# Kernel tuning notes

Hardware: AMD Instinct MI355X
Metric: run time of the kernel (lower is better)

Reference implementation:

```python
import jax, jax.numpy as jnp
import numpy as np

B, L, D, H, NL = 4, 1024, 1024, 16, 4
Dh = D // H          # 64 head dim
DFF = 4 * D          # GLU FFN hidden
EPS = 1e-5
NVARS = 64


def setup_inputs() -> dict:
    key = jax.random.key(0)
    ks = jax.random.split(key, 12)
    init = lambda k, shape, s=0.02: jax.random.normal(k, shape, jnp.float32) * s
    return dict(
        x=jax.random.normal(ks[0], (B, L, D), jnp.float32),
        var_id=jax.random.randint(ks[1], (B, L), 0, NVARS),
        positions=jnp.sort(jax.random.randint(ks[2], (B, L), 0, L), axis=-1),
        Wqkv=init(ks[3], (NL, D, 3 * D)),
        Wo=init(ks[4], (NL, D, D)),
        norm1_w=jnp.ones((NL, D), jnp.float32),
        norm2_w=jnp.ones((NL, D), jnp.float32),
        q_norm_w=jnp.ones((NL, Dh), jnp.float32),
        k_norm_w=jnp.ones((NL, Dh), jnp.float32),
        bias_emb=init(ks[5], (NL, 2, H), 0.1),  # BinaryAttentionBias per layer
        W_gate=init(ks[6], (NL, D, DFF)),
        W_up=init(ks[7], (NL, D, DFF)),
        W_down=init(ks[8], (NL, DFF, D)),
        final_norm_w=jnp.ones((D,), jnp.float32),
    )


def reference(x, var_id, positions, Wqkv, Wo, norm1_w, norm2_w, q_norm_w,
              k_norm_w, bias_emb, W_gate, W_up, W_down, final_norm_w):
    # var-equality mask for BinaryAttentionBias: [B,1,L,L]
    same = (var_id[:, :, None] == var_id[:, None, :])[:, None]
    # partial RoPE: rotary on first half of head_dim (partial_factor (0.0, 0.5))
    rot = Dh // 2
    inv_freq = jnp.exp(-jnp.log(10000.0) * jnp.arange(0, rot, 2, dtype=jnp.float32) / rot)
    theta = positions.astype(jnp.float32)[..., None] * inv_freq  # [B,L,rot/2]
    cos = jnp.cos(theta)[:, :, None, :]  # [B,L,1,rot/2]
    sin = jnp.sin(theta)[:, :, None, :]

    def rmsnorm(t, w):
        return t * jax.lax.rsqrt(jnp.mean(t * t, -1, keepdims=True) + EPS) * w

    def rope(t):  # t: [B,L,H,Dh]
        tr, tp = t[..., :rot], t[..., rot:]
        t1, t2 = tr[..., 0::2], tr[..., 1::2]
        rr = jnp.stack([t1 * cos - t2 * sin, t1 * sin + t2 * cos], -1).reshape(tr.shape)
        return jnp.concatenate([rr, tp], -1)

    scale = 1.0 / np.sqrt(Dh).astype(np.float32)

    def layer(h, p):
        Wqkv_l, Wo_l, n1, n2, qn, kn, be, Wg, Wu, Wd = p
        y = rmsnorm(h, n1)
        qkv = y @ Wqkv_l  # [B,L,3D]
        q, k, v = [a.reshape(B, L, H, Dh) for a in jnp.split(qkv, 3, axis=-1)]
        q = rope(rmsnorm(q, qn))  # qk-norm then rotary
        k = rope(rmsnorm(k, kn))
        bias = jnp.where(same, be[1][None, :, None, None], be[0][None, :, None, None])
        scores = jnp.einsum('blhd,bmhd->bhlm', q, k) * scale + bias
        attn = jax.nn.softmax(scores, axis=-1)
        o = jnp.einsum('bhlm,bmhd->blhd', attn, v).reshape(B, L, D)
        h = h + o @ Wo_l
        y = rmsnorm(h, n2)
        h = h + (jax.nn.silu(y @ Wg) * (y @ Wu)) @ Wd  # SiLU-GLU FFN
        return h, None

    params = (Wqkv, Wo, norm1_w, norm2_w, q_norm_w, k_norm_w, bias_emb,
              W_gate, W_up, W_down)
    h, _ = jax.lax.scan(layer, x, params)
    return rmsnorm(h, final_norm_w)
```

## Files before the change

### kernel.cpp

```cpp
#include <hip/hip_runtime.h>
#include <hip/hip_bf16.h>
#include <math.h>

#define B_   4
#define L_   1024
#define D_   1024
#define H_   16
#define NL_  4
#define DH_  64
#define DFF_ 4096
#define EPS_ 1e-5f

typedef unsigned short u16;
typedef __attribute__((ext_vector_type(8))) short short8;
typedef __attribute__((ext_vector_type(4))) float f32x4;

static __device__ __forceinline__ u16 f2bf(float x) {
  union { float f; unsigned u; } c;
  c.f = x;
  unsigned r = c.u + 0x7fffu + ((c.u >> 16) & 1u);
  return (u16)(r >> 16);
}
static __device__ __forceinline__ float bf2f(u16 x) {
  union { unsigned u; float f; } c;
  c.u = ((unsigned)x) << 16;
  return c.f;
}

__global__ __launch_bounds__(256) void transpose_cast_kernel(
    const float* __restrict__ W, u16* __restrict__ Wt, int R, int C) {
  __shared__ float tile[64][65];
  int r0 = blockIdx.y * 64, c0 = blockIdx.x * 64;
  int t = threadIdx.x;
#pragma unroll
  for (int i = 0; i < 4; i++) {
    int f = t + i * 256;
    int rr = f >> 4, c4 = f & 15;
    float4 v = *(const float4*)(W + (size_t)(r0 + rr) * C + c0 + c4 * 4);
    tile[rr][c4 * 4 + 0] = v.x;
    tile[rr][c4 * 4 + 1] = v.y;
    tile[rr][c4 * 4 + 2] = v.z;
    tile[rr][c4 * 4 + 3] = v.w;
  }
  __syncthreads();
#pragma unroll
  for (int i = 0; i < 4; i++) {
    int f = t + i * 256;
    int cc = f >> 4, rq = f & 15;
    unsigned p0 = (unsigned)f2bf(tile[rq * 4 + 0][cc]) |
                  ((unsigned)f2bf(tile[rq * 4 + 1][cc]) << 16);
    unsigned p1 = (unsigned)f2bf(tile[rq * 4 + 2][cc]) |
                  ((unsigned)f2bf(tile[rq * 4 + 3][cc]) << 16);
    uint2 q; q.x = p0; q.y = p1;
    *(uint2*)(Wt + (size_t)(c0 + cc) * R + r0 + rq * 4) = q;
  }
}

__global__ __launch_bounds__(256) void rmsnorm_kernel(
    const float* __restrict__ in, const float* __restrict__ w,
    float* __restrict__ out) {
  int row = blockIdx.x;
  const float4* x4 = (const float4*)(in + (size_t)row * D_);
  float4* y4 = (float4*)(out + (size_t)row * D_);
  const float4* w4 = (const float4*)w;
  int t = threadIdx.x;
  float4 v = x4[t];
  float ss = v.x * v.x + v.y * v.y + v.z * v.z + v.w * v.w;
#pragma unroll
  for (int off = 32; off > 0; off >>= 1) ss += __shfl_down(ss, off, 64);
  __shared__ float red[4];
  if ((t & 63) == 0) red[t >> 6] = ss;
  __syncthreads();
  float tot = red[0] + red[1] + red[2] + red[3];
  float r = rsqrtf(tot * (1.0f / D_) + EPS_);
  float4 wv = w4[t];
  float4 o;
  o.x = v.x * r * wv.x;
  o.y = v.y * r * wv.y;
  o.z = v.z * r * wv.z;
  o.w = v.w * r * wv.w;
  y4[t] = o;
}

__global__ __launch_bounds__(256) void rmsnorm_bf16_kernel(
    const float* __restrict__ in, const float* __restrict__ w,
    u16* __restrict__ out) {
  int row = blockIdx.x;
  const float4* x4 = (const float4*)(in + (size_t)row * D_);
  const float4* w4 = (const float4*)w;
  int t = threadIdx.x;
  float4 v = x4[t];
  float ss = v.x * v.x + v.y * v.y + v.z * v.z + v.w * v.w;
#pragma unroll
  for (int off = 32; off > 0; off >>= 1) ss += __shfl_down(ss, off, 64);
  __shared__ float red[4];
  if ((t & 63) == 0) red[t >> 6] = ss;
  __syncthreads();
  float tot = red[0] + red[1] + red[2] + red[3];
  float r = rsqrtf(tot * (1.0f / D_) + EPS_);
  float4 wv = w4[t];
  unsigned p0 = (unsigned)f2bf(v.x * r * wv.x) |
                ((unsigned)f2bf(v.y * r * wv.y) << 16);
  unsigned p1 = (unsigned)f2bf(v.z * r * wv.z) |
                ((unsigned)f2bf(v.w * r * wv.w) << 16);
  uint2 q; q.x = p0; q.y = p1;
  *(uint2*)(out + (size_t)row * D_ + t * 4) = q;
}

__global__ __launch_bounds__(256) void qknorm_rope_kernel(
    u16* __restrict__ qkv, const int* __restrict__ positions,
    const float* __restrict__ qn, const float* __restrict__ kn) {
  int tok = blockIdx.x;
  int p = blockIdx.y * 4 + (threadIdx.x >> 6);
  int d = threadIdx.x & 63;
  int isK = p >> 4;
  int h = p & 15;
  const float* w = isK ? kn : qn;
  u16* ptr = qkv + (size_t)tok * (3 * D_) + (size_t)isK * D_ + h * 64;
  float v = bf2f(ptr[d]);
  float ss = v * v;
#pragma unroll
  for (int off = 1; off < 64; off <<= 1) ss += __shfl_xor(ss, off, 64);
  float r = rsqrtf(ss * (1.0f / 64.0f) + EPS_);
  v = v * r * w[d];
  float pv = __shfl_xor(v, 1, 64);
  float outv = v;
  if (d < 32) {
    int i = d >> 1;
    float freq = __expf(-logf(10000.0f) * (float)(2 * i) * (1.0f / 32.0f));
    float th = (float)positions[tok] * freq;
    float s, c;
    __sincosf(th, &s, &c);
    outv = (d & 1) ? (pv * s + v * c) : (v * c - pv * s);
  }
  ptr[d] = f2bf(outv);
}

template <int MODE>
__global__ __launch_bounds__(256) void gemm_mfma(
    const u16* __restrict__ A, const u16* __restrict__ Bt,
    void* __restrict__ C, int M, int N, int K) {
  __shared__ u16 As[4096];
  __shared__ u16 Bs[4096];
  int t = threadIdx.x;
  int lane = t & 63, wv = t >> 6;
  int wm = wv >> 1, wn = wv & 1;
  int m0 = blockIdx.y * 128, n0 = blockIdx.x * 128;
  int lm = lane & 15, lk = lane >> 4;
  f32x4 acc[4][4];
#pragma unroll
  for (int i = 0; i < 4; i++)
#pragma unroll
    for (int j = 0; j < 4; j++) acc[i][j] = (f32x4)0.0f;

  for (int k0 = 0; k0 < K; k0 += 32) {
#pragma unroll
    for (int i = 0; i < 2; i++) {
      int s = wv * 2 + i;
      const u16* g = A + (size_t)(m0 + s * 16 + lm) * K + k0 + lk * 8;
      __builtin_amdgcn_global_load_lds(
          (const __attribute__((address_space(1))) void*)g,
          (__attribute__((address_space(3))) void*)(As + s * 512), 16, 0, 0);
    }
#pragma unroll
    for (int i = 0; i < 2; i++) {
      int s = wv * 2 + i;
      const u16* g = Bt + (size_t)(n0 + s * 16 + lm) * K + k0 + lk * 8;
      __builtin_amdgcn_global_load_lds(
          (const __attribute__((address_space(1))) void*)g,
          (__attribute__((address_space(3))) void*)(Bs + s * 512), 16, 0, 0);
    }
    __syncthreads();
    short8 a[4], b[4];
#pragma unroll
    for (int i = 0; i < 4; i++)
      a[i] = *(const short8*)(As + (wm * 4 + i) * 512 + lane * 8);
#pragma unroll
    for (int j = 0; j < 4; j++)
      b[j] = *(const short8*)(Bs + (wn * 4 + j) * 512 + lane * 8);
#pragma unroll
    for (int i = 0; i < 4; i++)
#pragma unroll
      for (int j = 0; j < 4; j++)
        acc[i][j] = __builtin_amdgcn_mfma_f32_16x16x32_bf16(
            a[i], b[j], acc[i][j], 0, 0, 0);
    __syncthreads();
  }

  int rb = (lane >> 4) * 4;
  int cl = lane & 15;
  size_t colbase = (size_t)(n0 + wn * 64 + cl);
#pragma unroll
  for (int i = 0; i < 4; i++) {
#pragma unroll
    for (int r = 0; r < 4; r++) {
      size_t row = (size_t)(m0 + wm * 64 + i * 16 + rb + r);
      if (MODE == 0) {
        float* p = (float*)C + row * N + colbase;
#pragma unroll
        for (int j = 0; j < 4; j++) p[j * 16] = acc[i][j][r];
      } else if (MODE == 1) {
        float* p = (float*)C + row * N + colbase;
#pragma unroll
        for (int j = 0; j < 4; j++) p[j * 16] += acc[i][j][r];
      } else if (MODE == 2) {
        u16* p = (u16*)C + row * N + colbase;
#pragma unroll
        for (int j = 0; j < 4; j++) p[j * 16] = f2bf(acc[i][j][r]);
      } else {
        u16* p = (u16*)C + row * N + colbase;
#pragma unroll
        for (int j = 0; j < 4; j++) {
          float g = acc[i][j][r];
          float u = bf2f(p[j * 16]);
          float sv = g / (1.0f + __expf(-g));
          p[j * 16] = f2bf(sv * u);
        }
      }
    }
  }
}

__global__ __launch_bounds__(256) void attn_mfma_kernel(
    const u16* __restrict__ qkv, const int* __restrict__ var_id,
    const float* __restrict__ bias_l, u16* __restrict__ o) {
  __shared__ u16 Ps[4][16 * 72];
  __shared__ u16 Vt[64 * 72];
  __shared__ int vks[64];
  int b = blockIdx.z, h = blockIdx.y, q0 = blockIdx.x * 64;
  int t = threadIdx.x, lane = t & 63, w = t >> 6;
  int cl = lane & 15, qd = lane >> 4;
  const size_t ROW = 3 * D_;
  const u16* qbase = qkv + (size_t)(b * L_) * ROW + h * 64;
  const u16* kbase = qbase + D_;
  const u16* vbase = qbase + 2 * D_;
  const float scale = 0.125f;

  int qrow = q0 + w * 16 + cl;
  short8 aq0 = *(const short8*)(qbase + (size_t)qrow * ROW + qd * 8);
  short8 aq1 = *(const short8*)(qbase + (size_t)qrow * ROW + 32 + qd * 8);

  int vq[4];
#pragma unroll
  for (int r = 0; r < 4; r++)
    vq[r] = var_id[b * L_ + q0 + w * 16 + qd * 4 + r];
  float b0 = bias_l[h], b1 = bias_l[H_ + h];

  float m_i[4], l_i[4];
  f32x4 oc[4];
#pragma unroll
  for (int r = 0; r < 4; r++) { m_i[r] = -1e30f; l_i[r] = 0.0f; }
#pragma unroll
  for (int ds = 0; ds < 4; ds++) oc[ds] = (f32x4)0.0f;

  int kp = t & 31, g = t >> 5;

  for (int kt = 0; kt < 16; kt++) {
    int k0 = kt * 64;
    {
      const u16* v0 = vbase + (size_t)(k0 + 2 * kp) * ROW + g * 8;
      short8 va = *(const short8*)v0;
      short8 vb = *(const short8*)(v0 + ROW);
#pragma unroll
      for (int j = 0; j < 8; j++) {
        unsigned pk = (unsigned)(u16)va[j] | ((unsigned)(u16)vb[j] << 16);
        *(unsigned*)&Vt[(g * 8 + j) * 72 + 2 * kp] = pk;
      }
      if (t < 64) vks[t] = var_id[b * L_ + k0 + t];
    }
    __syncthreads();

    f32x4 s[4];
#pragma unroll
    for (int j = 0; j < 4; j++) {
      const u16* kr = kbase + (size_t)(k0 + j * 16 + cl) * ROW;
      short8 bk0 = *(const short8*)(kr + qd * 8);
      short8 bk1 = *(const short8*)(kr + 32 + qd * 8);
      f32x4 a = (f32x4)0.0f;
      a = __builtin_amdgcn_mfma_f32_16x16x32_bf16(aq0, bk0, a, 0, 0, 0);
      a = __builtin_amdgcn_mfma_f32_16x16x32_bf16(aq1, bk1, a, 0, 0, 0);
      s[j] = a;
    }
#pragma unroll
    for (int j = 0; j < 4; j++) {
      int kv = vks[j * 16 + cl];
#pragma unroll
      for (int r = 0; r < 4; r++)
        s[j][r] = s[j][r] * scale + ((kv == vq[r]) ? b1 : b0);
    }
#pragma unroll
    for (int r = 0; r < 4; r++) {
      float rm = fmaxf(fmaxf(s[0][r], s[1][r]), fmaxf(s[2][r], s[3][r]));
#pragma unroll
      for (int off = 1; off < 16; off <<= 1)
        rm = fmaxf(rm, __shfl_xor(rm, off, 64));
      float mnew = fmaxf(m_i[r], rm);
      float alpha = __expf(m_i[r] - mnew);
      m_i[r] = mnew;
      float rs = 0.0f;
#pragma unroll
      for (int j = 0; j < 4; j++) {
        float p = __expf(s[j][r] - mnew);
        s[j][r] = p;
        rs += p;
      }
#pragma unroll
      for (int off = 1; off < 16; off <<= 1) rs += __shfl_xor(rs, off, 64);
      l_i[r] = l_i[r] * alpha + rs;
#pragma unroll
      for (int ds = 0; ds < 4; ds++) oc[ds][r] *= alpha;
    }
#pragma unroll
    for (int j = 0; j < 4; j++)
#pragma unroll
      for (int r = 0; r < 4; r++)
        Ps[w][(qd * 4 + r) * 72 + j * 16 + cl] = f2bf(s[j][r]);

    short8 ap0 = *(const short8*)(&Ps[w][cl * 72 + qd * 8]);
    short8 ap1 = *(const short8*)(&Ps[w][cl * 72 + 32 + qd * 8]);
#pragma unroll
    for (int ds = 0; ds < 4; ds++) {
      const u16* vr = &Vt[(ds * 16 + cl) * 72];
      short8 bv0 = *(const short8*)(vr + qd * 8);
      short8 bv1 = *(const short8*)(vr + 32 + qd * 8);
      oc[ds] = __builtin_amdgcn_mfma_f32_16x16x32_bf16(ap0, bv0, oc[ds], 0, 0, 0);
      oc[ds] = __builtin_amdgcn_mfma_f32_16x16x32_bf16(ap1, bv1, oc[ds], 0, 0, 0);
    }
    __syncthreads();
  }

#pragma unroll
  for (int r = 0; r < 4; r++) {
    float inv = 1.0f / l_i[r];
    size_t row = (size_t)(b * L_ + q0 + w * 16 + qd * 4 + r);
#pragma unroll
    for (int ds = 0; ds < 4; ds++)
      o[row * D_ + h * 64 + ds * 16 + cl] = f2bf(oc[ds][r] * inv);
  }
}

extern "C" void kernel_launch(void* const* d_in, const int* in_sizes, int n_in,
                              void* d_out, int out_size, void* d_ws,
                              size_t ws_size, hipStream_t stream) {
  (void)in_sizes; (void)n_in; (void)out_size; (void)ws_size;
  const float* x    = (const float*)d_in[0];
  const int* var_id = (const int*)d_in[1];
  const int* pos    = (const int*)d_in[2];
  const float* Wqkv = (const float*)d_in[3];
  const float* Wo   = (const float*)d_in[4];
  const float* n1   = (const float*)d_in[5];
  const float* n2   = (const float*)d_in[6];
  const float* qn   = (const float*)d_in[7];
  const float* kn   = (const float*)d_in[8];
  const float* be   = (const float*)d_in[9];
  const float* Wg   = (const float*)d_in[10];
  const float* Wu   = (const float*)d_in[11];
  const float* Wd   = (const float*)d_in[12];
  const float* fnw  = (const float*)d_in[13];

  float* h = (float*)d_out;
  const size_t MB = 1u << 20;
  char* wsb = (char*)d_ws;
  u16* y   = (u16*)(wsb);
  u16* qkv = (u16*)(wsb + 8*MB);
  u16* o   = (u16*)(wsb + 24*MB);
  u16* ff  = (u16*)(wsb + 32*MB);
  u16* wT  = (u16*)(wsb + 64*MB);
  u16* wqkvT = wT;
  u16* woT   = wqkvT + (size_t)3072*1024;
  u16* wgT   = woT   + (size_t)1024*1024;
  u16* wuT   = wgT   + (size_t)4096*1024;
  u16* wdT   = wuT   + (size_t)4096*1024;

  const size_t SZ = (size_t)B_ * L_ * D_;
  hipMemcpyAsync(h, x, SZ * sizeof(float), hipMemcpyDeviceToDevice, stream);

  const int M = B_ * L_;
  for (int l = 0; l < NL_; l++) {
    transpose_cast_kernel<<<dim3(48, 16), 256, 0, stream>>>(
        Wqkv + (size_t)l * D_ * 3 * D_, wqkvT, D_, 3 * D_);
    transpose_cast_kernel<<<dim3(16, 16), 256, 0, stream>>>(
        Wo + (size_t)l * D_ * D_, woT, D_, D_);
    transpose_cast_kernel<<<dim3(64, 16), 256, 0, stream>>>(
        Wg + (size_t)l * D_ * DFF_, wgT, D_, DFF_);
    transpose_cast_kernel<<<dim3(64, 16), 256, 0, stream>>>(
        Wu + (size_t)l * D_ * DFF_, wuT, D_, DFF_);
    transpose_cast_kernel<<<dim3(16, 64), 256, 0, stream>>>(
        Wd + (size_t)l * DFF_ * D_, wdT, DFF_, D_);

    rmsnorm_bf16_kernel<<<M, 256, 0, stream>>>(h, n1 + (size_t)l * D_, y);
    gemm_mfma<2><<<dim3(3 * D_ / 128, M / 128), 256, 0, stream>>>(
        y, wqkvT, qkv, M, 3 * D_, D_);
    qknorm_rope_kernel<<<dim3(M, 8), 256, 0, stream>>>(
        qkv, pos, qn + (size_t)l * DH_, kn + (size_t)l * DH_);
    attn_mfma_kernel<<<dim3(L_ / 64, H_, B_), 256, 0, stream>>>(
        qkv, var_id, be + (size_t)l * 2 * H_, o);
    gemm_mfma<1><<<dim3(D_ / 128, M / 128), 256, 0, stream>>>(
        o, woT, h, M, D_, D_);
    rmsnorm_bf16_kernel<<<M, 256, 0, stream>>>(h, n2 + (size_t)l * D_, y);
    gemm_mfma<2><<<dim3(DFF_ / 128, M / 128), 256, 0, stream>>>(
        y, wuT, ff, M, DFF_, D_);
    gemm_mfma<3><<<dim3(DFF_ / 128, M / 128), 256, 0, stream>>>(
        y, wgT, ff, M, DFF_, D_);
    gemm_mfma<1><<<dim3(D_ / 128, M / 128), 256, 0, stream>>>(
        ff, wdT, h, M, D_, DFF_);
  }
  rmsnorm_kernel<<<M, 256, 0, stream>>>(h, fnw, h);
}
```

Measured before the change: 2.295 ms.

## Register-prefetch GEMM tiles, fuse gate/up FFN GEMMs, shrink M-tile for narrow GEMMs

The GEMM kernel now loads the next K-slice into registers while the current slice is in LDS, replacing direct global-to-LDS loads, so memory latency overlaps with MFMA work. The gate and up projections are fused into one kernel that shares the A tile and applies SiLU*up in the epilogue, removing the second pass over y and the read-modify-write of ff. The N=1024 GEMMs (Wo, Wdown) use 64-row M tiles to launch more blocks. Costs are more registers (two 4x4 accumulator sets in the fused kernel) and possibly lower occupancy.

After: 4.411 ms. +92.2%, slower.

```diff
diff --git a/kernel.cpp b/kernel.cpp
--- a/kernel.cpp
+++ b/kernel.cpp
@@ -136,86 +136,190 @@
   ptr[d] = f2bf(outv);
 }
 
-template <int MODE>
+template <int MODE, int AI>
 __global__ __launch_bounds__(256) void gemm_mfma(
     const u16* __restrict__ A, const u16* __restrict__ Bt,
     void* __restrict__ C, int M, int N, int K) {
+  const int NA = AI / 2;
+  __shared__ u16 As[AI * 1024];
+  __shared__ u16 Bs[4096];
+  int t = threadIdx.x;
+  int lane = t & 63, wv = t >> 6;
+  int wm = wv >> 1, wn = wv & 1;
+  int m0 = blockIdx.y * (AI * 32), n0 = blockIdx.x * 128;
+  int lm = lane & 15, lk = lane >> 4;
+
+  const u16* pa[NA];
+  const u16* pb[2];
+#pragma unroll
+  for (int i = 0; i < NA; i++)
+    pa[i] = A + (size_t)(m0 + (wv * NA + i) * 16 + lm) * K + lk * 8;
+#pragma unroll
+  for (int i = 0; i < 2; i++)
+    pb[i] = Bt + (size_t)(n0 + (wv * 2 + i) * 16 + lm) * K + lk * 8;
+
+  uint4 ca[NA], cb[2];
+#pragma unroll
+  for (int i = 0; i < NA; i++) ca[i] = *(const uint4*)pa[i];
+#pragma unroll
+  for (int i = 0; i < 2; i++) cb[i] = *(const uint4*)pb[i];
+
+  f32x4 acc[AI][4];
+#pragma unroll
+  for (int i = 0; i < AI; i++)
+#pragma unroll
+    for (int j = 0; j < 4; j++) acc[i][j] = (f32x4)0.0f;
+
+  for (int k0 = 0; k0 < K; k0 += 32) {
+#pragma unroll
+    for (int i = 0; i < NA; i++)
+      *(uint4*)(As + (wv * NA + i) * 512 + lane * 8) = ca[i];
+#pragma unroll
+    for (int i = 0; i < 2; i++)
+      *(uint4*)(Bs + (wv * 2 + i) * 512 + lane * 8) = cb[i];
+    int kn = (k0 + 32 < K) ? (k0 + 32) : 0;
+    uint4 na[NA], nb[2];
+#pragma unroll
+    for (int i = 0; i < NA; i++) na[i] = *(const uint4*)(pa[i] + kn);
+#pragma unroll
+    for (int i = 0; i < 2; i++) nb[i] = *(const uint4*)(pb[i] + kn);
+    __syncthreads();
+    short8 a[AI], b[4];
+#pragma unroll
+    for (int i = 0; i < AI; i++)
+      a[i] = *(const short8*)(As + (wm * AI + i) * 512 + lane * 8);
+#pragma unroll
+    for (int j = 0; j < 4; j++)
+      b[j] = *(const short8*)(Bs + (wn * 4 + j) * 512 + lane * 8);
+#pragma unroll
+    for (int i = 0; i < AI; i++)
+#pragma unroll
+      for (int j = 0; j < 4; j++)
+        acc[i][j] = __builtin_amdgcn_mfma_f32_16x16x32_bf16(
+            a[i], b[j], acc[i][j], 0, 0, 0);
+    __syncthreads();
+#pragma unroll
+    for (int i = 0; i < NA; i++) ca[i] = na[i];
+#pragma unroll
+    for (int i = 0; i < 2; i++) cb[i] = nb[i];
+  }
+
+  int rb = (lane >> 4) * 4;
+  int cl = lane & 15;
+  size_t colbase = (size_t)(n0 + wn * 64 + cl);
+#pragma unroll
+  for (int i = 0; i < AI; i++) {
+#pragma unroll
+    for (int r = 0; r < 4; r++) {
+      size_t row = (size_t)(m0 + wm * (AI * 16) + i * 16 + rb + r);
+      if (MODE == 1) {
+        float* p = (float*)C + row * N + colbase;
+#pragma unroll
+        for (int j = 0; j < 4; j++) p[j * 16] += acc[i][j][r];
+      } else {
+        u16* p = (u16*)C + row * N + colbase;
+#pragma unroll
+        for (int j = 0; j < 4; j++) p[j * 16] = f2bf(acc[i][j][r]);
+      }
+    }
+  }
+}
+
+__global__ __launch_bounds__(256) void gemm_dff_fused(
+    const u16* __restrict__ A, const u16* __restrict__ WgT,
+    const u16* __restrict__ WuT, u16* __restrict__ ff, int M) {
+  const int K = D_;
   __shared__ u16 As[4096];
-  __shared__ u16 Bs[4096];
+  __shared__ u16 Gs[4096];
+  __shared__ u16 Us[4096];
   int t = threadIdx.x;
   int lane = t & 63, wv = t >> 6;
   int wm = wv >> 1, wn = wv & 1;
   int m0 = blockIdx.y * 128, n0 = blockIdx.x * 128;
   int lm = lane & 15, lk = lane >> 4;
-  f32x4 acc[4][4];
+
+  const u16* pa[2];
+  const u16* pg[2];
+  const u16* pu[2];
+#pragma unroll
+  for (int i = 0; i < 2; i++) {
+    int s = wv * 2 + i;
+    pa[i] = A + (size_t)(m0 + s * 16 + lm) * K + lk * 8;
+    pg[i] = WgT + (size_t)(n0 + s * 16 + lm) * K + lk * 8;
+    pu[i] = WuT + (size_t)(n0 + s * 16 + lm) * K + lk * 8;
+  }
+  uint4 ca[2], cg[2], cu[2];
+#pragma unroll
+  for (int i = 0; i < 2; i++) {
+    ca[i] = *(const uint4*)pa[i];
+    cg[i] = *(const uint4*)pg[i];
+    cu[i] = *(const uint4*)pu[i];
+  }
+
+  f32x4 accg[4][4], accu[4][4];
 #pragma unroll
   for (int i = 0; i < 4; i++)
 #pragma unroll
-    for (int j = 0; j < 4; j++) acc[i][j] = (f32x4)0.0f;
+    for (int j = 0; j < 4; j++) {
+      accg[i][j] = (f32x4)0.0f;
+      accu[i][j] = (f32x4)0.0f;
+    }
 
   for (int k0 = 0; k0 < K; k0 += 32) {
 #pragma unroll
     for (int i = 0; i < 2; i++) {
       int s = wv * 2 + i;
-      const u16* g = A + (size_t)(m0 + s * 16 + lm) * K + k0 + lk * 8;
-      __builtin_amdgcn_global_load_lds(
-          (const __attribute__((address_space(1))) void*)g,
-          (__attribute__((address_space(3))) void*)(As + s * 512), 16, 0, 0);
-    }
+      *(uint4*)(As + s * 512 + lane * 8) = ca[i];
+      *(uint4*)(Gs + s * 512 + lane * 8) = cg[i];
+      *(uint4*)(Us + s * 512 + lane * 8) = cu[i];
+    }
+    int kn = (k0 + 32 < K) ? (k0 + 32) : 0;
+    uint4 na[2], ng[2], nu[2];
 #pragma unroll
     for (int i = 0; i < 2; i++) {
-      int s = wv * 2 + i;
-      const u16* g = Bt + (size_t)(n0 + s * 16 + lm) * K + k0 + lk * 8;
-      __builtin_amdgcn_global_load_lds(
-          (const __attribute__((address_space(1))) void*)g,
-          (__attribute__((address_space(3))) void*)(Bs + s * 512), 16, 0, 0);
+      na[i] = *(const uint4*)(pa[i] + kn);
+      ng[i] = *(const uint4*)(pg[i] + kn);
+      nu[i] = *(const uint4*)(pu[i] + kn);
     }
     __syncthreads();
-    short8 a[4], b[4];
+    short8 a[4], g[4], u[4];
+#pragma unroll
+    for (int i = 0; i < 4; i++) {
+      a[i] = *(const short8*)(As + (wm * 4 + i) * 512 + lane * 8);
+      g[i] = *(const short8*)(Gs + (wn * 4 + i) * 512 + lane * 8);
+      u[i] = *(const short8*)(Us + (wn * 4 + i) * 512 + lane * 8);
+    }
 #pragma unroll
     for (int i = 0; i < 4; i++)
-      a[i] = *(const short8*)(As + (wm * 4 + i) * 512 + lane * 8);
-#pragma unroll
-    for (int j = 0; j < 4; j++)
-      b[j] = *(const short8*)(Bs + (wn * 4 + j) * 512 + lane * 8);
-#pragma unroll
-    for (int i = 0; i < 4; i++)
-#pragma unroll
-      for (int j = 0; j < 4; j++)
-        acc[i][j] = __builtin_amdgcn_mfma_f32_16x16x32_bf16(
-            a[i], b[j], acc[i][j], 0, 0, 0);
+#pragma unroll
+      for (int j = 0; j < 4; j++) {
+        accg[i][j] = __builtin_amdgcn_mfma_f32_16x16x32_bf16(
+            a[i], g[j], accg[i][j], 0, 0, 0);
+        accu[i][j] = __builtin_amdgcn_mfma_f32_16x16x32_bf16(
+            a[i], u[j], accu[i][j], 0, 0, 0);
+      }
     __syncthreads();
+#pragma unroll
+    for (int i = 0; i < 2; i++) {
+      ca[i] = na[i];
+      cg[i] = ng[i];
+      cu[i] = nu[i];
+    }
   }
 
   int rb = (lane >> 4) * 4;
   int cl = lane & 15;
-  size_t colbase = (size_t)(n0 + wn * 64 + cl);
 #pragma unroll
   for (int i = 0; i < 4; i++) {
 #pragma unroll
     for (int r = 0; r < 4; r++) {
       size_t row = (size_t)(m0 + wm * 64 + i * 16 + rb + r);
-      if (MODE == 0) {
-        float* p = (float*)C + row * N + colbase;
-#pragma unroll
-        for (int j = 0; j < 4; j++) p[j * 16] = acc[i][j][r];
-      } else if (MODE == 1) {
-        float* p = (float*)C + row * N + colbase;
-#pragma unroll
-        for (int j = 0; j < 4; j++) p[j * 16] += acc[i][j][r];
-      } else if (MODE == 2) {
-        u16* p = (u16*)C + row * N + colbase;
-#pragma unroll
-        for (int j = 0; j < 4; j++) p[j * 16] = f2bf(acc[i][j][r]);
-      } else {
-        u16* p = (u16*)C + row * N + colbase;
-#pragma unroll
-        for (int j = 0; j < 4; j++) {
-          float g = acc[i][j][r];
-          float u = bf2f(p[j * 16]);
-          float sv = g / (1.0f + __expf(-g));
-          p[j * 16] = f2bf(sv * u);
-        }
+      u16* p = ff + row * DFF_ + n0 + wn * 64 + cl;
+#pragma unroll
+      for (int j = 0; j < 4; j++) {
+        float gg = accg[i][j][r];
+        float uu = accu[i][j][r];
+        p[j * 16] = f2bf((gg / (1.0f + __expf(-gg))) * uu);
       }
     }
   }
@@ -389,20 +493,18 @@
         Wd + (size_t)l * DFF_ * D_, wdT, DFF_, D_);
 
     rmsnorm_bf16_kernel<<<M, 256, 0, stream>>>(h, n1 + (size_t)l * D_, y);
-    gemm_mfma<2><<<dim3(3 * D_ / 128, M / 128), 256, 0, stream>>>(
+    gemm_mfma<2, 4><<<dim3(3 * D_ / 128, M / 128), 256, 0, stream>>>(
         y, wqkvT, qkv, M, 3 * D_, D_);
     qknorm_rope_kernel<<<dim3(M, 8), 256, 0, stream>>>(
         qkv, pos, qn + (size_t)l * DH_, kn + (size_t)l * DH_);
     attn_mfma_kernel<<<dim3(L_ / 64, H_, B_), 256, 0, stream>>>(
         qkv, var_id, be + (size_t)l * 2 * H_, o);
-    gemm_mfma<1><<<dim3(D_ / 128, M / 128), 256, 0, stream>>>(
+    gemm_mfma<1, 2><<<dim3(D_ / 128, M / 64), 256, 0, stream>>>(
         o, woT, h, M, D_, D_);
     rmsnorm_bf16_kernel<<<M, 256, 0, stream>>>(h, n2 + (size_t)l * D_, y);
-    gemm_mfma<2><<<dim3(DFF_ / 128, M / 128), 256, 0, stream>>>(
-        y, wuT, ff, M, DFF_, D_);
-    gemm_mfma<3><<<dim3(DFF_ / 128, M / 128), 256, 0, stream>>>(
-        y, wgT, ff, M, DFF_, D_);
-    gemm_mfma<1><<<dim3(D_ / 128, M / 128), 256, 0, stream>>>(
+    gemm_dff_fused<<<dim3(DFF_ / 128, M / 128), 256, 0, stream>>>(
+        y, wgT, wuT, ff, M);
+    gemm_mfma<1, 2><<<dim3(D_ / 128, M / 64), 256, 0, stream>>>(
         ff, wdT, h, M, D_, DFF_);
   }
   rmsnorm_kernel<<<M, 256, 0, stream>>>(h, fnw, h);
```
